# Kernel optimization log

Hardware: AMD Instinct MI355X
Metric: run time of the kernel (lower is better)

The kernel has to match this reference:

```python
import jax, jax.numpy as jnp
import numpy as np

N_NODES = 50000
N_EDGES = 1600000
N_REL = 8
D_IN = 128
D_HID = 128
D_OUT = 64
N_POOL = 256


def setup_inputs() -> dict:
    key = jax.random.key(0)
    ks = jax.random.split(key, 10)
    x = jax.random.uniform(ks[0], (N_NODES, D_IN), dtype=jnp.float32)
    edge_index = jax.random.randint(ks[1], (2, N_EDGES), 0, N_NODES)
    edge_type = jax.random.randint(ks[2], (N_EDGES,), 0, N_REL)
    pool_indices = jax.random.randint(ks[3], (N_POOL,), 0, N_NODES)
    s1 = 1.0 / np.sqrt(D_IN)
    s2 = 1.0 / np.sqrt(D_HID)
    W1 = jax.random.normal(ks[4], (N_REL, D_IN, D_HID), dtype=jnp.float32) * s1
    root1 = jax.random.normal(ks[5], (D_IN, D_HID), dtype=jnp.float32) * s1
    b1 = jnp.zeros((D_HID,), jnp.float32)
    W2 = jax.random.normal(ks[6], (N_REL, D_HID, D_OUT), dtype=jnp.float32) * s2
    root2 = jax.random.normal(ks[7], (D_HID, D_OUT), dtype=jnp.float32) * s2
    b2 = jnp.zeros((D_OUT,), jnp.float32)
    return {"x": x, "edge_index": edge_index, "edge_type": edge_type,
            "pool_indices": pool_indices, "W1": W1, "root1": root1, "b1": b1,
            "W2": W2, "root2": root2, "b2": b2}


def rgcn_layer(h, edge_index, edge_type, W, root, b):
    # PyG RGCNConv: out = h @ root + sum_r mean_{j in N_r(i)} (h_j @ W_r) + b
    src, dst = edge_index[0], edge_index[1]
    n = h.shape[0]
    r = W.shape[0]
    hW = jnp.einsum('nd,rdh->rnh', h, W)          # (R, N, H)
    msg = hW[edge_type, src]                      # (E, H) gather per edge
    seg = edge_type * n + dst                     # per-(relation, dst) segment
    agg = jax.ops.segment_sum(msg, seg, num_segments=r * n)
    agg = agg.reshape(r, n, -1)
    cnt = jax.ops.segment_sum(jnp.ones(msg.shape[0], h.dtype), seg,
                              num_segments=r * n).reshape(r, n, 1)
    mean = agg / jnp.maximum(cnt, 1.0)            # per-relation mean
    return mean.sum(0) + h @ root + b


def reference(x, edge_index, edge_type, pool_indices, W1, root1, b1, W2, root2, b2):
    h = jax.nn.relu(rgcn_layer(x, edge_index, edge_type, W1, root1, b1))
    node_embeddings = rgcn_layer(h, edge_index, edge_type, W2, root2, b2)
    selected_embeddings = node_embeddings[pool_indices]       # (P, D_OUT)
    type_features = x[pool_indices, :3]                       # (P, 3)
    weights = jnp.array([4.0, 1.0, 2.0], dtype=x.dtype)
    entity_weights = type_features @ weights                  # (P,)
    sum_of_weights = jnp.sum(entity_weights) + 1e-9
    pooled = jnp.sum(selected_embeddings * entity_weights[:, None], axis=0,
                     keepdims=True) / sum_of_weights          # (1, D_OUT)
    return pooled
```

## Files before the change

kernel.cpp:

```cpp
#include <hip/hip_runtime.h>

#define N_NODES 50000
#define N_EDGES 1600000
#define N_REL   8
#define D_IN    128
#define D_HID   128
#define D_OUT   64
#define N_POOL  256

#define CAP_S   12288
#define BUCKET  32
#define BUCKET2 32
#define NSEG_N  (N_REL * N_NODES)

typedef short v8s __attribute__((ext_vector_type(8)));
typedef float v4f __attribute__((ext_vector_type(4)));

constexpr size_t OFF_FILLC  = 0;
constexpr size_t OFF_FILLC2 = OFF_FILLC + NSEG_N;
constexpr size_t ZERO_ELEMS = OFF_FILLC2 + NSEG_N;
constexpr size_t OFF_PBIT   = ZERO_ELEMS;
constexpr size_t OFF_SBIT   = OFF_PBIT + 2048;
constexpr size_t OFF_CTR    = OFF_SBIT + 2048;
constexpr size_t OFF_SNODES = OFF_CTR + 16;
constexpr size_t OFF_SRCSLOT= OFF_SNODES + CAP_S;
constexpr size_t OFF_ESLOT2 = OFF_SRCSLOT + (size_t)NSEG_N * BUCKET;
constexpr size_t OFF_AGG1B  = OFF_ESLOT2 + (size_t)NSEG_N * BUCKET2;
constexpr size_t OFF_XALL   = OFF_AGG1B + (size_t)NSEG_N * 64;
constexpr size_t OFF_WT     = OFF_XALL + (size_t)N_NODES * 64;
constexpr size_t OFF_H      = OFF_WT + (size_t)1152 * 128 / 2;
constexpr size_t OFF_EMB    = OFF_H + (size_t)N_NODES * D_HID;
constexpr size_t TOTAL_ELEMS= OFF_EMB + (size_t)N_POOL * D_OUT;

__device__ __forceinline__ unsigned short f2bf(float f) {
  union { float f; unsigned u; } v; v.f = f;
  unsigned r = v.u + 0x7FFFu + ((v.u >> 16) & 1u);
  return (unsigned short)(r >> 16);
}
__device__ __forceinline__ float bfLo(unsigned v) { return __uint_as_float(v << 16); }
__device__ __forceinline__ float bfHi(unsigned v) { return __uint_as_float(v & 0xFFFF0000u); }

__global__ __launch_bounds__(256) void k_init(
    const int* __restrict__ pool, const float* __restrict__ x,
    const float* __restrict__ W1, const float* __restrict__ root1,
    float* __restrict__ ws) {
  unsigned* pBit = (unsigned*)(ws + OFF_PBIT);
  unsigned* sBit = (unsigned*)(ws + OFF_SBIT);
  int*      ctr  = (int*)(ws + OFF_CTR);
  unsigned long long* xall8 = (unsigned long long*)(ws + OFF_XALL);
  unsigned short* Wt = (unsigned short*)(ws + OFF_WT);
  int tid = threadIdx.x, bid = blockIdx.x;
  int gtid = bid * 256 + tid, gthr = gridDim.x * 256;
  int wave = tid >> 6, lane = tid & 63;

  float4 z = {0.f, 0.f, 0.f, 0.f};
  for (int i = gtid; i < (int)(ZERO_ELEMS / 4); i += gthr) ((float4*)ws)[i] = z;

  if (bid == 0) {
    for (int i = tid; i < 2048; i += 256) { pBit[i] = 0u; sBit[i] = 0u; }
    if (tid < 16) ctr[tid] = 0;
    __syncthreads();
    int node = pool[tid];
    unsigned bit = 1u << (node & 31);
    atomicOr(&pBit[node >> 5], bit);
    atomicOr(&sBit[node >> 5], bit);
  }

  int gw = (bid - 1) * 4 + wave;
  if (bid >= 1 && gw < 288) {
    int kt = gw >> 3, nt = gw & 7;
    int k0 = kt * 32 + ((lane >> 4) << 3);
    int n = nt * 16 + (lane & 15);
    v8s frag;
#pragma unroll
    for (int j = 0; j < 8; j++) {
      int kg = k0 + j;
      float v = (kg < 1024) ? W1[(size_t)kg * D_HID + n]
                            : root1[(size_t)(kg - 1024) * D_HID + n];
      frag[j] = (short)f2bf(v);
    }
    ((v8s*)Wt)[gw * 64 + lane] = frag;
  }

  for (int i = gtid; i < N_NODES * 32; i += gthr) {
    float4 v = ((const float4*)x)[i];
    unsigned lo = ((unsigned)f2bf(v.y) << 16) | f2bf(v.x);
    unsigned hi = ((unsigned)f2bf(v.w) << 16) | f2bf(v.z);
    xall8[i] = (unsigned long long)lo | ((unsigned long long)hi << 32);
  }
}

__global__ __launch_bounds__(256) void k_pass1(
    const int* __restrict__ EI, const int* __restrict__ pool,
    unsigned* __restrict__ sBit) {
  __shared__ unsigned pb[2048];
  int tid = threadIdx.x;
  for (int i = tid; i < 2048; i += 256) pb[i] = 0u;
  __syncthreads();
  { int node = pool[tid]; atomicOr(&pb[node >> 5], 1u << (node & 31)); }
  __syncthreads();
  int idx = blockIdx.x * 256 + tid;
  if (idx >= N_EDGES / 4) return;
  int4 d4 = ((const int4*)(EI + N_EDGES))[idx];
  int d[4] = {d4.x, d4.y, d4.z, d4.w};
#pragma unroll
  for (int i = 0; i < 4; i++) {
    int dst = d[i];
    if ((pb[dst >> 5] >> (dst & 31)) & 1u) {
      int src = EI[idx * 4 + i];
      atomicOr(&sBit[src >> 5], 1u << (src & 31));
    }
  }
}

__global__ __launch_bounds__(256) void k_fillc(
    const int* __restrict__ EI, const int* __restrict__ ET,
    const int* __restrict__ pool, const unsigned* __restrict__ sBit,
    int* __restrict__ fillCtr, int* __restrict__ srcSlot,
    int* __restrict__ fillCtr2, int* __restrict__ eslot2,
    int* __restrict__ sNodes, int* __restrict__ ctr) {
  __shared__ unsigned pb[2048];
  __shared__ int ismem[8];
  int tid = threadIdx.x, bid = blockIdx.x;
  int wave = tid >> 6, lane = tid & 63;
  for (int i = tid; i < 2048; i += 256) pb[i] = 0u;
  __syncthreads();
  { int node = pool[tid]; atomicOr(&pb[node >> 5], 1u << (node & 31)); }
  __syncthreads();

  if (bid < 196) {
    int node = bid * 256 + tid;
    bool sp = (node < N_NODES) && ((sBit[node >> 5] >> (node & 31)) & 1u);
    unsigned long long m = __ballot(sp);
    if (lane == 0) ismem[wave] = __popcll(m);
    __syncthreads();
    if (tid == 0) {
      int tot = ismem[0] + ismem[1] + ismem[2] + ismem[3];
      ismem[4] = tot ? atomicAdd(&ctr[1], tot) : 0;
    }
    __syncthreads();
    if (sp) {
      int off = ismem[4];
      for (int w2 = 0; w2 < wave; w2++) off += ismem[w2];
      int id = off + __popcll(m & ((1ull << lane) - 1ull));
      if (id < CAP_S) sNodes[id] = node;
    }
  }

  int idx = bid * 256 + tid;
  if (idx >= N_EDGES / 4) return;
  int4 d4 = ((const int4*)(EI + N_EDGES))[idx];
  int d[4] = {d4.x, d4.y, d4.z, d4.w};
  bool any = false;
#pragma unroll
  for (int i = 0; i < 4; i++)
    any |= ((sBit[d[i] >> 5] >> (d[i] & 31)) & 1u) != 0u;
  if (!any) return;
  int4 t4 = ((const int4*)ET)[idx];
  int4 s4 = ((const int4*)EI)[idx];
  int t[4] = {t4.x, t4.y, t4.z, t4.w};
  int s[4] = {s4.x, s4.y, s4.z, s4.w};
#pragma unroll
  for (int i = 0; i < 4; i++) {
    int dst = d[i];
    if ((sBit[dst >> 5] >> (dst & 31)) & 1u) {
      int seg = (dst << 3) + t[i];
      int slot = atomicAdd(&fillCtr[seg], 1);
      if (slot < BUCKET) srcSlot[(size_t)seg * BUCKET + slot] = s[i];
      if ((pb[dst >> 5] >> (dst & 31)) & 1u) {
        int slot2 = atomicAdd(&fillCtr2[seg], 1);
        if (slot2 < BUCKET2) eslot2[(size_t)seg * BUCKET2 + slot2] = s[i];
      }
    }
  }
}

__global__ __launch_bounds__(256) void k_gather(
    const int* __restrict__ fillCtr, const int* __restrict__ srcSlot,
    const unsigned* __restrict__ xall, const int* __restrict__ ctr,
    const int* __restrict__ sNodes, unsigned* __restrict__ agg1b) {
  int sCount = ctr[1]; if (sCount > CAP_S) sCount = CAP_S;
  int total = sCount << 3;
  int lane = threadIdx.x & 63;
  int wstride = gridDim.x << 2;
  for (int w = (blockIdx.x << 2) + (threadIdx.x >> 6); w < total; w += wstride) {
    int node = sNodes[w >> 3];
    int seg = (node << 3) + (w & 7);
    int cnt = fillCtr[seg];
    if (cnt > BUCKET) cnt = BUCKET;
    const int* slot = srcSlot + (size_t)seg * BUCKET;
    float a0 = 0.f, a1 = 0.f;
    int i = 0;
    for (; i + 4 <= cnt; i += 4) {
      int s0 = slot[i + 0];
      int s1 = slot[i + 1];
      int s2 = slot[i + 2];
      int s3 = slot[i + 3];
      unsigned v0 = xall[(size_t)s0 * 64 + lane];
      unsigned v1 = xall[(size_t)s1 * 64 + lane];
      unsigned v2 = xall[(size_t)s2 * 64 + lane];
      unsigned v3 = xall[(size_t)s3 * 64 + lane];
      a0 += (bfLo(v0) + bfLo(v1)) + (bfLo(v2) + bfLo(v3));
      a1 += (bfHi(v0) + bfHi(v1)) + (bfHi(v2) + bfHi(v3));
    }
    for (; i < cnt; i++) {
      unsigned v = xall[(size_t)slot[i] * 64 + lane];
      a0 += bfLo(v);
      a1 += bfHi(v);
    }
    float inv = 1.0f / fmaxf((float)cnt, 1.0f);
    agg1b[(size_t)seg * 64 + lane] = ((unsigned)f2bf(a1 * inv) << 16) | f2bf(a0 * inv);
  }
}

__global__ __launch_bounds__(256) void k_gemm1(
    const unsigned* __restrict__ agg1b, const unsigned* __restrict__ xall,
    const unsigned short* __restrict__ Wt, const float* __restrict__ b1,
    const int* __restrict__ sNodes, const int* __restrict__ ctr,
    float* __restrict__ h) {
  int sCount = ctr[1]; if (sCount > CAP_S) sCount = CAP_S;
  int s0 = blockIdx.x * 16;
  if (s0 >= sCount) return;
  int wave = threadIdx.x >> 6, lane = threadIdx.x & 63;
  int quad = lane >> 4, mn = lane & 15;
  int srow = s0 + mn;
  int g = (srow < sCount) ? sNodes[srow] : 0;
  v4f acc0 = (v4f){0.f, 0.f, 0.f, 0.f};
  v4f acc1 = (v4f){0.f, 0.f, 0.f, 0.f};
  const v8s* WtF = (const v8s*)Wt;
  for (int kt = 0; kt < 36; kt++) {
    const unsigned short* aptr;
    if (kt < 32) {
      int r = kt >> 2;
      int d0 = (kt & 3) * 32 + quad * 8;
      aptr = (const unsigned short*)agg1b + ((size_t)((g << 3) + r) * 128 + d0);
    } else {
      int d0 = (kt - 32) * 32 + quad * 8;
      aptr = (const unsigned short*)xall + ((size_t)g * 128 + d0);
    }
    v8s afrag = *(const v8s*)aptr;
    const v8s* wrow = WtF + (size_t)(kt * 8 + wave * 2) * 64 + lane;
    acc0 = __builtin_amdgcn_mfma_f32_16x16x32_bf16(afrag, wrow[0],  acc0, 0, 0, 0);
    acc1 = __builtin_amdgcn_mfma_f32_16x16x32_bf16(afrag, wrow[64], acc1, 0, 0, 0);
  }
  int col0 = wave * 32 + mn;
  int col1 = col0 + 16;
  float bv0 = b1[col0], bv1 = b1[col1];
#pragma unroll
  for (int reg = 0; reg < 4; reg++) {
    int s = s0 + quad * 4 + reg;
    if (s < sCount) {
      int gh = sNodes[s];
      h[(size_t)gh * D_HID + col0] = fmaxf(acc0[reg] + bv0, 0.0f);
      h[(size_t)gh * D_HID + col1] = fmaxf(acc1[reg] + bv1, 0.0f);
    }
  }
}

__global__ __launch_bounds__(256) void k_gemmB(
    const float* __restrict__ x, const int* __restrict__ pool,
    const float* __restrict__ W2, const float* __restrict__ root2,
    const float* __restrict__ b2, const int* __restrict__ fillCtr2,
    const int* __restrict__ eslot2, int* __restrict__ ctr,
    const float* __restrict__ h, float* __restrict__ emb,
    float* __restrict__ out) {
  __shared__ float smem[1408];
  __shared__ int lastFlag;
  int tid = threadIdx.x, wave = tid >> 6, lane = tid & 63;
  int pl = blockIdx.x;
  {
    int nodeP = pool[pl];
    float* a = smem;
    float* partial = smem + 1152;
#pragma unroll
    for (int rr = 0; rr < 2; rr++) {
      int r = wave * 2 + rr;
      int code = (nodeP << 3) + r;
      int cnt = fillCtr2[code]; if (cnt > BUCKET2) cnt = BUCKET2;
      const int* sl = eslot2 + (size_t)code * BUCKET2;
      float s0 = 0.f, s1 = 0.f;
      for (int i = 0; i < cnt; i++) {
        float2 v = ((const float2*)h)[(size_t)sl[i] * 64 + lane];
        s0 += v.x; s1 += v.y;
      }
      float inv = 1.0f / fmaxf((float)cnt, 1.0f);
      a[r * 128 + lane * 2]     = s0 * inv;
      a[r * 128 + lane * 2 + 1] = s1 * inv;
    }
    if (tid < 128) a[1024 + tid] = h[(size_t)nodeP * D_HID + tid];
    __syncthreads();
    int lo = wave * 288, hi = lo + 288;
    float acc = 0.0f;
    int hiW = (hi < 1024) ? hi : 1024;
#pragma unroll 8
    for (int k = lo; k < hiW; k++) acc += a[k] * W2[(size_t)k * D_OUT + lane];
    int loR = (lo > 1024) ? lo : 1024;
#pragma unroll 8
    for (int k = loR; k < hi; k++) acc += a[k] * root2[(size_t)(k - 1024) * D_OUT + lane];
    partial[tid] = acc;
    __syncthreads();
    if (tid < 64) {
      float r4 = partial[tid] + partial[tid + 64] + partial[tid + 128] + partial[tid + 192];
      emb[(size_t)pl * D_OUT + tid] = r4 + b2[tid];
    }
  }
  __syncthreads();
  if (tid == 0) {
    __builtin_amdgcn_fence(__ATOMIC_RELEASE, "agent");
    int old = __hip_atomic_fetch_add(&ctr[2], 1, __ATOMIC_RELAXED,
                                     __HIP_MEMORY_SCOPE_AGENT);
    lastFlag = (old == (int)gridDim.x - 1) ? 1 : 0;
  }
  __syncthreads();
  if (lastFlag == 0) return;
  if (tid == 0) __builtin_amdgcn_fence(__ATOMIC_ACQUIRE, "agent");
  __syncthreads();
  {
    float* ew  = smem;
    float* part= smem + 512;
    int node = pool[tid];
    const float* xr = x + (size_t)node * D_IN;
    ew[tid] = 4.0f * xr[0] + 1.0f * xr[1] + 2.0f * xr[2];
    __syncthreads();
    float acc = 0.0f;
    int j0 = wave * 64;
#pragma unroll 8
    for (int j = j0; j < j0 + 64; j++)
      acc += ew[j] * emb[(size_t)j * D_OUT + lane];
    part[wave * 64 + lane] = acc;
    __syncthreads();
    if (tid < 64) {
      float sw = 0.0f;
      for (int j = 0; j < N_POOL; j++) sw += ew[j];
      float r4 = part[tid] + part[64 + tid] + part[128 + tid] + part[192 + tid];
      out[tid] = r4 / (sw + 1e-9f);
    }
  }
}

extern "C" void kernel_launch(void* const* d_in, const int* in_sizes, int n_in,
                              void* d_out, int out_size, void* d_ws, size_t ws_size,
                              hipStream_t stream) {
  const float* x     = (const float*)d_in[0];
  const int*   EI    = (const int*)  d_in[1];
  const int*   ET    = (const int*)  d_in[2];
  const int*   pool  = (const int*)  d_in[3];
  const float* W1    = (const float*)d_in[4];
  const float* root1 = (const float*)d_in[5];
  const float* b1    = (const float*)d_in[6];
  const float* W2    = (const float*)d_in[7];
  const float* root2 = (const float*)d_in[8];
  const float* b2    = (const float*)d_in[9];
  float* out = (float*)d_out;
  float* ws  = (float*)d_ws;

  int*      fillCtr = (int*)(ws + OFF_FILLC);
  int*      fillCtr2= (int*)(ws + OFF_FILLC2);
  unsigned* sBit    = (unsigned*)(ws + OFF_SBIT);
  int*      ctr     = (int*)(ws + OFF_CTR);
  int*      sNodes  = (int*)(ws + OFF_SNODES);
  int*      srcSlot = (int*)(ws + OFF_SRCSLOT);
  int*      eslot2  = (int*)(ws + OFF_ESLOT2);
  unsigned* agg1b   = (unsigned*)(ws + OFF_AGG1B);
  unsigned* xall    = (unsigned*)(ws + OFF_XALL);
  unsigned short* Wt = (unsigned short*)(ws + OFF_WT);
  float*    h       = ws + OFF_H;
  float*    emb     = ws + OFF_EMB;

  k_init<<<1024, 256, 0, stream>>>(pool, x, W1, root1, ws);
  k_pass1<<<(N_EDGES / 4 + 255) / 256, 256, 0, stream>>>(EI, pool, sBit);
  k_fillc<<<(N_EDGES / 4 + 255) / 256, 256, 0, stream>>>(
      EI, ET, pool, sBit, fillCtr, srcSlot, fillCtr2, eslot2, sNodes, ctr);
  k_gather<<<4096, 256, 0, stream>>>(fillCtr, srcSlot, xall, ctr, sNodes, agg1b);
  k_gemm1<<<CAP_S / 16, 256, 0, stream>>>(agg1b, xall, Wt, b1, sNodes, ctr, h);
  k_gemmB<<<N_POOL, 256, 0, stream>>>(
      x, pool, W2, root2, b2, fillCtr2, eslot2, ctr, h, emb, out);
}
```

Before: 185.3 us.

## Widen gather loads to 64-bit and split layer-2 GEMM across two blocks per pool node

Measured after the change: 176.0 us, median of 2. -5.0%, faster.

```diff
diff --git a/kernel.cpp b/kernel.cpp
--- a/kernel.cpp
+++ b/kernel.cpp
@@ -49,12 +49,14 @@
   int*      ctr  = (int*)(ws + OFF_CTR);
   unsigned long long* xall8 = (unsigned long long*)(ws + OFF_XALL);
   unsigned short* Wt = (unsigned short*)(ws + OFF_WT);
+  float4*   emb4 = (float4*)(ws + OFF_EMB);
   int tid = threadIdx.x, bid = blockIdx.x;
   int gtid = bid * 256 + tid, gthr = gridDim.x * 256;
   int wave = tid >> 6, lane = tid & 63;
 
   float4 z = {0.f, 0.f, 0.f, 0.f};
   for (int i = gtid; i < (int)(ZERO_ELEMS / 4); i += gthr) ((float4*)ws)[i] = z;
+  for (int i = gtid; i < N_POOL * D_OUT / 4; i += gthr) emb4[i] = z;
 
   if (bid == 0) {
     for (int i = tid; i < 2048; i += 256) { pBit[i] = 0u; sBit[i] = 0u; }
@@ -177,39 +179,53 @@
 
 __global__ __launch_bounds__(256) void k_gather(
     const int* __restrict__ fillCtr, const int* __restrict__ srcSlot,
-    const unsigned* __restrict__ xall, const int* __restrict__ ctr,
-    const int* __restrict__ sNodes, unsigned* __restrict__ agg1b) {
+    const unsigned long long* __restrict__ xall8, const int* __restrict__ ctr,
+    const int* __restrict__ sNodes, unsigned long long* __restrict__ agg1b8) {
   int sCount = ctr[1]; if (sCount > CAP_S) sCount = CAP_S;
   int total = sCount << 3;
   int lane = threadIdx.x & 63;
+  int half = lane >> 5, hl = lane & 31;
   int wstride = gridDim.x << 2;
-  for (int w = (blockIdx.x << 2) + (threadIdx.x >> 6); w < total; w += wstride) {
-    int node = sNodes[w >> 3];
-    int seg = (node << 3) + (w & 7);
-    int cnt = fillCtr[seg];
-    if (cnt > BUCKET) cnt = BUCKET;
-    const int* slot = srcSlot + (size_t)seg * BUCKET;
-    float a0 = 0.f, a1 = 0.f;
-    int i = 0;
-    for (; i + 4 <= cnt; i += 4) {
-      int s0 = slot[i + 0];
-      int s1 = slot[i + 1];
-      int s2 = slot[i + 2];
-      int s3 = slot[i + 3];
-      unsigned v0 = xall[(size_t)s0 * 64 + lane];
-      unsigned v1 = xall[(size_t)s1 * 64 + lane];
-      unsigned v2 = xall[(size_t)s2 * 64 + lane];
-      unsigned v3 = xall[(size_t)s3 * 64 + lane];
-      a0 += (bfLo(v0) + bfLo(v1)) + (bfLo(v2) + bfLo(v3));
-      a1 += (bfHi(v0) + bfHi(v1)) + (bfHi(v2) + bfHi(v3));
-    }
-    for (; i < cnt; i++) {
-      unsigned v = xall[(size_t)slot[i] * 64 + lane];
-      a0 += bfLo(v);
-      a1 += bfHi(v);
-    }
-    float inv = 1.0f / fmaxf((float)cnt, 1.0f);
-    agg1b[(size_t)seg * 64 + lane] = ((unsigned)f2bf(a1 * inv) << 16) | f2bf(a0 * inv);
+  for (int p = (blockIdx.x << 2) + (threadIdx.x >> 6); 2 * p < total; p += wstride) {
+    int w = 2 * p + half;
+    if (w < total) {
+      int node = sNodes[w >> 3];
+      int seg = (node << 3) + (w & 7);
+      int cnt = fillCtr[seg];
+      if (cnt > BUCKET) cnt = BUCKET;
+      const int* slot = srcSlot + (size_t)seg * BUCKET;
+      float a0 = 0.f, a1 = 0.f, a2 = 0.f, a3 = 0.f;
+      int i = 0;
+      for (; i + 4 <= cnt; i += 4) {
+        int s0 = slot[i + 0];
+        int s1 = slot[i + 1];
+        int s2 = slot[i + 2];
+        int s3 = slot[i + 3];
+        unsigned long long v0 = xall8[(size_t)s0 * 32 + hl];
+        unsigned long long v1 = xall8[(size_t)s1 * 32 + hl];
+        unsigned long long v2 = xall8[(size_t)s2 * 32 + hl];
+        unsigned long long v3 = xall8[(size_t)s3 * 32 + hl];
+        unsigned l0 = (unsigned)v0, h0 = (unsigned)(v0 >> 32);
+        unsigned l1 = (unsigned)v1, h1 = (unsigned)(v1 >> 32);
+        unsigned l2 = (unsigned)v2, h2 = (unsigned)(v2 >> 32);
+        unsigned l3 = (unsigned)v3, h3 = (unsigned)(v3 >> 32);
+        a0 += (bfLo(l0) + bfLo(l1)) + (bfLo(l2) + bfLo(l3));
+        a1 += (bfHi(l0) + bfHi(l1)) + (bfHi(l2) + bfHi(l3));
+        a2 += (bfLo(h0) + bfLo(h1)) + (bfLo(h2) + bfLo(h3));
+        a3 += (bfHi(h0) + bfHi(h1)) + (bfHi(h2) + bfHi(h3));
+      }
+      for (; i < cnt; i++) {
+        unsigned long long v = xall8[(size_t)slot[i] * 32 + hl];
+        unsigned lo = (unsigned)v, hi = (unsigned)(v >> 32);
+        a0 += bfLo(lo); a1 += bfHi(lo);
+        a2 += bfLo(hi); a3 += bfHi(hi);
+      }
+      float inv = 1.0f / fmaxf((float)cnt, 1.0f);
+      unsigned w0 = ((unsigned)f2bf(a1 * inv) << 16) | f2bf(a0 * inv);
+      unsigned w1 = ((unsigned)f2bf(a3 * inv) << 16) | f2bf(a2 * inv);
+      agg1b8[(size_t)seg * 32 + hl] =
+          (unsigned long long)w0 | ((unsigned long long)w1 << 32);
+    }
   }
 }
 
@@ -264,44 +280,45 @@
     const int* __restrict__ eslot2, int* __restrict__ ctr,
     const float* __restrict__ h, float* __restrict__ emb,
     float* __restrict__ out) {
-  __shared__ float smem[1408];
+  __shared__ float smem[896];
   __shared__ int lastFlag;
   int tid = threadIdx.x, wave = tid >> 6, lane = tid & 63;
-  int pl = blockIdx.x;
+  int pl = blockIdx.x >> 1, half = blockIdx.x & 1;
   {
     int nodeP = pool[pl];
     float* a = smem;
-    float* partial = smem + 1152;
-#pragma unroll
-    for (int rr = 0; rr < 2; rr++) {
-      int r = wave * 2 + rr;
-      int code = (nodeP << 3) + r;
-      int cnt = fillCtr2[code]; if (cnt > BUCKET2) cnt = BUCKET2;
-      const int* sl = eslot2 + (size_t)code * BUCKET2;
-      float s0 = 0.f, s1 = 0.f;
-      for (int i = 0; i < cnt; i++) {
-        float2 v = ((const float2*)h)[(size_t)sl[i] * 64 + lane];
-        s0 += v.x; s1 += v.y;
-      }
-      float inv = 1.0f / fmaxf((float)cnt, 1.0f);
-      a[r * 128 + lane * 2]     = s0 * inv;
-      a[r * 128 + lane * 2 + 1] = s1 * inv;
-    }
-    if (tid < 128) a[1024 + tid] = h[(size_t)nodeP * D_HID + tid];
-    __syncthreads();
-    int lo = wave * 288, hi = lo + 288;
+    float* partial = smem + 640;
+    int r = half * 4 + wave;
+    int code = (nodeP << 3) + r;
+    int cnt = fillCtr2[code]; if (cnt > BUCKET2) cnt = BUCKET2;
+    const int* sl = eslot2 + (size_t)code * BUCKET2;
+    float s0 = 0.f, s1 = 0.f;
+    for (int i = 0; i < cnt; i++) {
+      float2 v = ((const float2*)h)[(size_t)sl[i] * 64 + lane];
+      s0 += v.x; s1 += v.y;
+    }
+    float inv = 1.0f / fmaxf((float)cnt, 1.0f);
+    a[wave * 128 + lane * 2]     = s0 * inv;
+    a[wave * 128 + lane * 2 + 1] = s1 * inv;
+    if (half == 1 && tid < 128) a[512 + tid] = h[(size_t)nodeP * D_HID + tid];
+    __syncthreads();
     float acc = 0.0f;
-    int hiW = (hi < 1024) ? hi : 1024;
+    int kbase = half * 512 + wave * 128;
 #pragma unroll 8
-    for (int k = lo; k < hiW; k++) acc += a[k] * W2[(size_t)k * D_OUT + lane];
-    int loR = (lo > 1024) ? lo : 1024;
-#pragma unroll 8
-    for (int k = loR; k < hi; k++) acc += a[k] * root2[(size_t)(k - 1024) * D_OUT + lane];
+    for (int j = 0; j < 128; j++)
+      acc += a[wave * 128 + j] * W2[(size_t)(kbase + j) * D_OUT + lane];
+    if (half == 1) {
+      int rbase = wave * 32;
+#pragma unroll 4
+      for (int j = 0; j < 32; j++)
+        acc += a[512 + rbase + j] * root2[(size_t)(rbase + j) * D_OUT + lane];
+    }
     partial[tid] = acc;
     __syncthreads();
     if (tid < 64) {
       float r4 = partial[tid] + partial[tid + 64] + partial[tid + 128] + partial[tid + 192];
-      emb[(size_t)pl * D_OUT + tid] = r4 + b2[tid];
+      if (half == 0) r4 += b2[tid];
+      unsafeAtomicAdd(&emb[(size_t)pl * D_OUT + tid], r4);
     }
   }
   __syncthreads();
@@ -371,8 +388,10 @@
   k_pass1<<<(N_EDGES / 4 + 255) / 256, 256, 0, stream>>>(EI, pool, sBit);
   k_fillc<<<(N_EDGES / 4 + 255) / 256, 256, 0, stream>>>(
       EI, ET, pool, sBit, fillCtr, srcSlot, fillCtr2, eslot2, sNodes, ctr);
-  k_gather<<<4096, 256, 0, stream>>>(fillCtr, srcSlot, xall, ctr, sNodes, agg1b);
+  k_gather<<<4096, 256, 0, stream>>>(
+      fillCtr, srcSlot, (const unsigned long long*)xall, ctr, sNodes,
+      (unsigned long long*)agg1b);
   k_gemm1<<<CAP_S / 16, 256, 0, stream>>>(agg1b, xall, Wt, b1, sNodes, ctr, h);
-  k_gemmB<<<N_POOL, 256, 0, stream>>>(
+  k_gemmB<<<2 * N_POOL, 256, 0, stream>>>(
       x, pool, W2, root2, b2, fillCtr2, eslot2, ctr, h, emb, out);
 }
```
